# Performance work log

Hardware: AMD Instinct MI355X
Metric: run time of the kernel (lower is better)

Reference implementation:

```python
import jax, jax.numpy as jnp
import numpy as np

EPS = 1e-8
LN_EPS = 1e-5
PSCALE = 10.0
P = 8  # n_points


def _bb_frames(Xn, Xca, Xc):
    # Gram-Schmidt rigid frame from N, CA, C (AlphaFold rigids_from_3_points).
    v1 = Xc - Xca
    v2 = Xn - Xca
    e1 = v1 / jnp.sqrt(jnp.sum(v1 * v1, -1, keepdims=True) + EPS)
    u2 = v2 - e1 * jnp.sum(e1 * v2, -1, keepdims=True)
    e2 = u2 / jnp.sqrt(jnp.sum(u2 * u2, -1, keepdims=True) + EPS)
    e3 = jnp.cross(e1, e2)
    R = jnp.stack([e1, e2, e3], axis=-1)  # [B,N,3,3], columns are basis vectors
    t = Xca / PSCALE                      # scale_translation(1/position_scale)
    return R, t


def _layernorm(x, g, b):
    mu = jnp.mean(x, -1, keepdims=True)
    var = jnp.mean((x - mu) ** 2, -1, keepdims=True)
    return (x - mu) / jnp.sqrt(var + LN_EPS) * g + b


def setup_inputs() -> dict:
    key = jax.random.key(0)
    ks = jax.random.split(key, 24)
    B, N, K, D, H = 8, 512, 32, 128, 128
    msg_in = 2 * D + D + 9 * P  # 456
    s = 0.02
    inp = {
        "h_V": jax.random.normal(ks[0], (B, N, D), jnp.float32),
        "h_E": jax.random.normal(ks[1], (B, N, K, D), jnp.float32),
        "X": jax.random.normal(ks[2], (B, N, 3, 3), jnp.float32),
        "mask_V": jnp.ones((B, N), jnp.float32),
        "mask_attend": jnp.ones((B, N, K), jnp.float32),
        "Wp": jax.random.normal(ks[3], (D, P * 3), jnp.float32) * s,
        "bp": jnp.zeros((P * 3,), jnp.float32),
        "Wm1": jax.random.normal(ks[4], (msg_in, H), jnp.float32) * s,
        "bm1": jnp.zeros((H,), jnp.float32),
        "Wm2": jax.random.normal(ks[5], (H, H), jnp.float32) * s,
        "bm2": jnp.zeros((H,), jnp.float32),
        "Wm3": jax.random.normal(ks[6], (H, H), jnp.float32) * s,
        "bm3": jnp.zeros((H,), jnp.float32),
        "g1": jnp.ones((H,), jnp.float32),
        "be1": jnp.zeros((H,), jnp.float32),
        "Wd1": jax.random.normal(ks[7], (H, 4 * H), jnp.float32) * s,
        "bd1": jnp.zeros((4 * H,), jnp.float32),
        "Wd2": jax.random.normal(ks[8], (4 * H, H), jnp.float32) * s,
        "bd2": jnp.zeros((H,), jnp.float32),
        "g2": jnp.ones((H,), jnp.float32),
        "be2": jnp.zeros((H,), jnp.float32),
        "E_idx": jax.random.randint(ks[9], (B, N, K), 0, N, jnp.int32),
    }
    return inp


def reference(h_V, h_E, X, mask_V, mask_attend,
              Wp, bp, Wm1, bm1, Wm2, bm2, Wm3, bm3, g1, be1,
              Wd1, bd1, Wd2, bd2, g2, be2, E_idx):
    B, N, K = E_idx.shape
    R, t = _bb_frames(X[..., 0, :], X[..., 1, :], X[..., 2, :])
    # local points [B,N,P,3]
    p_local = (h_V @ Wp + bp).reshape(B, N, P, 3)
    # global points: R @ p + t
    p_global = jnp.einsum('bnij,bnpj->bnpi', R, p_local) + t[:, :, None, :]
    bidx = jnp.arange(B)[:, None, None]
    nbr_pg = p_global[bidx, E_idx]  # [B,N,K,P,3]
    nbr_hV = h_V[bidx, E_idx]       # [B,N,K,D]
    # distances in global frame
    diff = p_global[:, :, None] - nbr_pg
    npg_norm = jnp.sqrt(jnp.sum(diff * diff, -1) + EPS)  # [B,N,K,P]
    # neighbor points in local frame: R^T (q - t)
    q = nbr_pg - t[:, :, None, None, :]
    nbr_pl = jnp.einsum('bnij,bnkpi->bnkpj', R, q)       # [B,N,K,P,3]
    npl_norm = jnp.sqrt(jnp.sum(nbr_pl * nbr_pl, -1) + EPS)
    pl_norm = jnp.sqrt(jnp.sum(p_local * p_local, -1) + EPS)  # [B,N,P]

    D = h_V.shape[-1]
    node_expand = jnp.broadcast_to(h_V[:, :, None, :], (B, N, K, D))
    pl_flat = jnp.broadcast_to(p_local[:, :, None], (B, N, K, P, 3)).reshape(B, N, K, P * 3)
    pl_norm_e = jnp.broadcast_to(pl_norm[:, :, None, :], (B, N, K, P))
    msg_in = jnp.concatenate([
        node_expand, h_E, nbr_hV,
        pl_flat, pl_norm_e,
        nbr_pl.reshape(B, N, K, P * 3), npl_norm, npg_norm,
    ], axis=-1)

    # node_message_fn: 3-layer MLP with relu
    m = jax.nn.relu(msg_in @ Wm1 + bm1)
    m = jax.nn.relu(m @ Wm2 + bm2)
    m = m @ Wm3 + bm3
    m = m * mask_attend[..., None]
    node_m = jnp.mean(m, axis=-2)  # [B,N,H]

    h = _layernorm(h_V + node_m, g1, be1)  # dropout = identity (eval)
    dense = jax.nn.relu(h @ Wd1 + bd1) @ Wd2 + bd2
    h = _layernorm(h + dense, g2, be2)
    h = h * mask_V[..., None]
    return h, h_E
```

## Files before the change

### kernel.cpp

```cpp
#include <hip/hip_runtime.h>
#include <hip/hip_bf16.h>

typedef __hip_bfloat16 bf16;
typedef __attribute__((ext_vector_type(8))) short s16x8;
typedef __attribute__((ext_vector_type(4))) float f32x4;

#define DEV __device__ __forceinline__

DEV float us2f(unsigned short u){ return __uint_as_float(((unsigned int)u) << 16); }
DEV unsigned short f2us(float f){
    __hip_bfloat16 h = __float2bfloat16(f);
    unsigned short r; __builtin_memcpy(&r, &h, 2); return r;
}
DEV unsigned pack2(float a, float b){ return (unsigned)f2us(a) | ((unsigned)f2us(b) << 16); }

template<bool F32> DEV float ldf(const void* p, long i){
    if (F32) return reinterpret_cast<const float*>(p)[i];
    return us2f(reinterpret_cast<const unsigned short*>(p)[i]);
}
template<bool F32> DEV unsigned short ld16(const void* p, long i){
    if (F32) return f2us(reinterpret_cast<const float*>(p)[i]);
    return reinterpret_cast<const unsigned short*>(p)[i];
}

union U16x8 { uint4 u; s16x8 v; };

DEV bool is_f32(const void* maskV){
    return reinterpret_cast<const unsigned short*>(maskV)[0] != 0x3F80;
}

struct __align__(16) PreSmem {
    union __align__(16) {
        unsigned short lwT[128*40];
        struct {
            unsigned short lwp[24*132];
            float sX[2][9], sR[2][9], st3[2][3], spl[2][24], hvs[2][128];
        } pr;
    } u;
};

template<bool F32>
DEV void pre_prep(const void* hV, const void* X, const void* Wp, const void* bp,
                  float* pg, float* pl, float* pln, float* Rw, float* tw,
                  PreSmem& s, int bid, int tid)
{
    auto& pr = s.u.pr;
    for (int e = tid; e < 3072; e += 128) {
        int i = e / 24, j = e - i*24;
        pr.lwp[j*132 + i] = ld16<F32>(Wp, e);
    }
    const int wv = tid >> 6, ln = tid & 63;
    const int n = bid*2 + wv;
    if (ln < 9) pr.sX[wv][ln] = ldf<F32>(X, (long)n*9 + ln);
    for (int i = ln; i < 128; i += 64) pr.hvs[wv][i] = ldf<F32>(hV, (long)n*128 + i);
    __syncthreads();

    if (ln == 0) {
        float Nx=pr.sX[wv][0],Ny=pr.sX[wv][1],Nz=pr.sX[wv][2];
        float Ax=pr.sX[wv][3],Ay=pr.sX[wv][4],Az=pr.sX[wv][5];
        float Cx=pr.sX[wv][6],Cy=pr.sX[wv][7],Cz=pr.sX[wv][8];
        float v1x=Cx-Ax, v1y=Cy-Ay, v1z=Cz-Az;
        float v2x=Nx-Ax, v2y=Ny-Ay, v2z=Nz-Az;
        float r1 = 1.f/sqrtf(v1x*v1x+v1y*v1y+v1z*v1z + 1e-8f);
        float e1x=v1x*r1, e1y=v1y*r1, e1z=v1z*r1;
        float dp = e1x*v2x+e1y*v2y+e1z*v2z;
        float u2x=v2x-e1x*dp, u2y=v2y-e1y*dp, u2z=v2z-e1z*dp;
        float r2 = 1.f/sqrtf(u2x*u2x+u2y*u2y+u2z*u2z + 1e-8f);
        float e2x=u2x*r2, e2y=u2y*r2, e2z=u2z*r2;
        float e3x = e1y*e2z - e1z*e2y;
        float e3y = e1z*e2x - e1x*e2z;
        float e3z = e1x*e2y - e1y*e2x;
        pr.sR[wv][0]=e1x; pr.sR[wv][1]=e2x; pr.sR[wv][2]=e3x;
        pr.sR[wv][3]=e1y; pr.sR[wv][4]=e2y; pr.sR[wv][5]=e3y;
        pr.sR[wv][6]=e1z; pr.sR[wv][7]=e2z; pr.sR[wv][8]=e3z;
        pr.st3[wv][0]=Ax*0.1f; pr.st3[wv][1]=Ay*0.1f; pr.st3[wv][2]=Az*0.1f;
    }
    if (ln < 24) {
        float acc = ldf<F32>(bp, ln);
        const unsigned short* wr = &pr.lwp[ln*132];
        #pragma unroll
        for (int c=0;c<16;c++){
            #pragma unroll
            for (int k=0;k<8;k++)
                acc += pr.hvs[wv][c*8+k] * us2f(wr[c*8+k]);
        }
        pr.spl[wv][ln] = acc;
    }
    __syncthreads();

    if (ln < 24) {
        pl[n*24+ln] = pr.spl[wv][ln];
        int p = ln/3, c = ln - p*3;
        float g = pr.sR[wv][c*3+0]*pr.spl[wv][p*3+0] + pr.sR[wv][c*3+1]*pr.spl[wv][p*3+1]
                + pr.sR[wv][c*3+2]*pr.spl[wv][p*3+2] + pr.st3[wv][c];
        pg[n*24+ln] = g;
    }
    if (ln < 9) Rw[n*9+ln] = pr.sR[wv][ln];
    if (ln < 3) tw[n*3+ln] = pr.st3[wv][ln];
    if (ln < 8) {
        float a=pr.spl[wv][ln*3], b=pr.spl[wv][ln*3+1], c=pr.spl[wv][ln*3+2];
        pln[n*8+ln] = sqrtf(a*a+b*b+c*c + 1e-8f);
    }
}

template<bool F32>
DEV void pre_uv(const void* hV, const void* bm1, const void* Wm1,
                unsigned short* Uw, unsigned short* Vw,
                PreSmem& s, int r0, int tid)
{
    const int lane = tid & 63, w2 = tid >> 6;
    const int lm = lane & 15, quad = lane >> 4;

    s16x8 af[4];
    #pragma unroll
    for (int kc=0; kc<4; ++kc) {
        long src = (long)(r0 + lm)*128 + kc*32 + quad*8;
        U16x8 pk;
        if (F32) {
            const float4* vp = reinterpret_cast<const float4*>(reinterpret_cast<const float*>(hV) + src);
            float4 x = vp[0], y = vp[1];
            pk.u.x = pack2(x.x,x.y); pk.u.y = pack2(x.z,x.w);
            pk.u.z = pack2(y.x,y.y); pk.u.w = pack2(y.z,y.w);
        } else {
            pk.u = *reinterpret_cast<const uint4*>(reinterpret_cast<const unsigned short*>(hV) + src);
        }
        af[kc] = pk.v;
    }

    f32x4 accU[4], accV[4];
    #pragma unroll
    for (int nt=0; nt<4; ++nt) {
        float b0 = ldf<F32>(bm1, 64*w2 + nt*16 + lm);
        f32x4 iv = {b0,b0,b0,b0};
        accU[nt] = iv;
        f32x4 zv = {0.f,0.f,0.f,0.f};
        accV[nt] = zv;
    }

    for (int p=0; p<8; ++p) {
        int k0 = (p<4) ? p*32 : 256 + (p-4)*32;
        __syncthreads();
        for (int e = tid; e < 4096; e += 128) {
            int kk = e >> 7, c = e & 127;
            s.u.lwT[c*40 + kk] = ld16<F32>(Wm1, (long)k0*128 + e);
        }
        __syncthreads();
        s16x8 a = af[p & 3];
        #pragma unroll
        for (int nt=0; nt<4; ++nt) {
            s16x8 bf = *reinterpret_cast<const s16x8*>(&s.u.lwT[(64*w2 + nt*16 + lm)*40 + quad*8]);
            if (p < 4) accU[nt] = __builtin_amdgcn_mfma_f32_16x16x32_bf16(a, bf, accU[nt], 0,0,0);
            else       accV[nt] = __builtin_amdgcn_mfma_f32_16x16x32_bf16(a, bf, accV[nt], 0,0,0);
        }
    }
    #pragma unroll
    for (int nt=0; nt<4; ++nt)
        #pragma unroll
        for (int r=0; r<4; ++r) {
            long o = (long)(r0 + quad*4 + r)*128 + 64*w2 + nt*16 + lm;
            Uw[o] = f2us(accU[nt][r]);
            Vw[o] = f2us(accV[nt][r]);
        }
}

template<bool F32>
DEV void pre_wt(const void* Wm1, const void* Wm2, const void* Wm3,
                const void* Wd1, const void* Wd2,
                unsigned short* wt1, unsigned short* wt2, unsigned short* wt3,
                unsigned short* wd1T, unsigned short* wd2T, long t)
{
    if (t < 61440) {
        int k = (int)(t >> 7), h = (int)(t & 127);
        wt1[(long)h*480 + k] = (k < 456) ? ld16<F32>(Wm1, (long)k*128 + h) : (unsigned short)0;
    } else if (t < 77824) {
        long t2 = t - 61440; int k = (int)(t2 >> 7), h = (int)(t2 & 127);
        wt2[(long)h*128 + k] = ld16<F32>(Wm2, (long)k*128 + h);
    } else if (t < 94208) {
        long t2 = t - 77824; int k = (int)(t2 >> 7), h = (int)(t2 & 127);
        wt3[(long)h*128 + k] = ld16<F32>(Wm3, (long)k*128 + h);
    } else if (t < 159744) {
        long t2 = t - 94208; int k = (int)(t2 >> 9), n = (int)(t2 & 511);
        wd1T[(long)n*128 + k] = ld16<F32>(Wd1, (long)k*512 + n);
    } else {
        long t2 = t - 159744; int k = (int)(t2 >> 7), n = (int)(t2 & 127);
        wd2T[(long)n*512 + k] = ld16<F32>(Wd2, (long)k*128 + n);
    }
}

__global__ __launch_bounds__(128) void pre_k(
    const void* __restrict__ hV, const void* __restrict__ X,
    const void* __restrict__ Wp, const void* __restrict__ bp,
    const void* __restrict__ Wm1, const void* __restrict__ bm1,
    const void* __restrict__ Wm2, const void* __restrict__ Wm3,
    const void* __restrict__ Wd1, const void* __restrict__ Wd2,
    float* __restrict__ pg, float* __restrict__ pl, float* __restrict__ pln,
    float* __restrict__ Rw, float* __restrict__ tw,
    unsigned short* __restrict__ Uw, unsigned short* __restrict__ Vw,
    unsigned short* __restrict__ wt1, unsigned short* __restrict__ wt2,
    unsigned short* __restrict__ wt3, unsigned short* __restrict__ wd1T,
    unsigned short* __restrict__ wd2T, const void* __restrict__ maskV)
{
    __shared__ PreSmem s;
    int bid = blockIdx.x, tid = threadIdx.x;
    bool f32 = is_f32(maskV);
    if (bid < 2048) {
        if (f32) pre_prep<true >(hV,X,Wp,bp,pg,pl,pln,Rw,tw,s,bid,tid);
        else     pre_prep<false>(hV,X,Wp,bp,pg,pl,pln,Rw,tw,s,bid,tid);
    } else if (bid < 2304) {
        int r0 = (bid - 2048) * 16;
        if (f32) pre_uv<true >(hV,bm1,Wm1,Uw,Vw,s,r0,tid);
        else     pre_uv<false>(hV,bm1,Wm1,Uw,Vw,s,r0,tid);
    } else {
        long t = (long)(bid - 2304)*128 + tid;
        if (f32) pre_wt<true >(Wm1,Wm2,Wm3,Wd1,Wd2,wt1,wt2,wt3,wd1T,wd2T,t);
        else     pre_wt<false>(Wm1,Wm2,Wm3,Wd1,Wd2,wt1,wt2,wt3,wd1T,wd2T,t);
    }
}

#define ASTRIDE 40
#define MSTRIDE 136

struct __align__(16) Mp1Smem {
    union __align__(16) {
        unsigned short geo[3][64*ASTRIDE];
        unsigned short m[64*MSTRIDE];
    } u;
    int   sj[64];
    float smka[64];
    float spg[2][24], spl[2][24], spln[2][8], sR[2][9], st3[2][3];
    unsigned short sU[2*128];
};

template<bool F32>
DEV void mpnn1_body(
    const void* hV, const void* hE, const void* maskA,
    const void* bm2, const void* bm3, const int* Eidx,
    const float* pg, const float* pl, const float* pln,
    const float* Rw, const float* tw,
    const unsigned short* wt1, const unsigned short* wt2, const unsigned short* wt3,
    const unsigned short* Uw, const unsigned short* Vw,
    float* nodemsg, void* outE, Mp1Smem& sm, int n0, int tid)
{
    const int lane = tid & 63, w = tid >> 6;
    const int lm = lane & 15, quad = lane >> 4;

    if (tid < 64) { int l = tid >> 5;
        sm.sj[tid] = (((n0+l) >> 9) << 9) + Eidx[(long)(n0+l)*32 + (tid & 31)];
    } else { int t = tid - 64; int l = t >> 5;
        sm.smka[t] = ldf<F32>(maskA, (long)(n0+l)*32 + (t & 31));
    }
    if (tid < 48)        { sm.spg[tid/24][tid%24] = pg[(n0+tid/24)*24 + tid%24]; }
    else if (tid < 96)   { int t=tid-48; sm.spl[t/24][t%24] = pl[(n0+t/24)*24 + t%24]; }
    else if (tid < 112)  { int t=tid-96; sm.spln[t>>3][t&7]  = pln[(n0+(t>>3))*8 + (t&7)]; }
    if (tid < 18)        { sm.sR[tid/9][tid%9] = Rw[(n0+tid/9)*9 + tid%9]; }
    else if (tid < 24)   { int t=tid-18; sm.st3[t/3][t%3] = tw[(n0+t/3)*3 + t%3]; }
    for (int e = tid; e < 256; e += 128)
        sm.sU[e] = Uw[(long)(n0 + (e>>7))*128 + (e & 127)];
    __syncthreads();

    #pragma unroll
    for (int pass=0; pass<4; ++pass) {
        int v = tid + pass*128;
        int row = v >> 3, p = v & 7, nd = row >> 5;
        int j = sm.sj[row];
        float qx = pg[j*24 + p*3 + 0];
        float qy = pg[j*24 + p*3 + 1];
        float qz = pg[j*24 + p*3 + 2];
        float dx = sm.spg[nd][p*3+0]-qx, dy = sm.spg[nd][p*3+1]-qy, dz = sm.spg[nd][p*3+2]-qz;
        float npg = sqrtf(dx*dx+dy*dy+dz*dz + 1e-8f);
        float ux = qx - sm.st3[nd][0], uy = qy - sm.st3[nd][1], uz = qz - sm.st3[nd][2];
        float l0 = sm.sR[nd][0]*ux + sm.sR[nd][3]*uy + sm.sR[nd][6]*uz;
        float l1 = sm.sR[nd][1]*ux + sm.sR[nd][4]*uy + sm.sR[nd][7]*uz;
        float l2v= sm.sR[nd][2]*ux + sm.sR[nd][5]*uy + sm.sR[nd][8]*uz;
        float npl = sqrtf(l0*l0+l1*l1+l2v*l2v + 1e-8f);
        unsigned short* C0 = sm.u.geo[0];
        unsigned short* C1 = sm.u.geo[1];
        unsigned short* C2 = sm.u.geo[2];
        C0[row*ASTRIDE + p*3+0] = f2us(sm.spl[nd][p*3+0]);
        C0[row*ASTRIDE + p*3+1] = f2us(sm.spl[nd][p*3+1]);
        C0[row*ASTRIDE + p*3+2] = f2us(sm.spl[nd][p*3+2]);
        C0[row*ASTRIDE + 24+p]  = f2us(sm.spln[nd][p]);
        C1[row*ASTRIDE + p*3+0] = f2us(l0);
        C1[row*ASTRIDE + p*3+1] = f2us(l1);
        C1[row*ASTRIDE + p*3+2] = f2us(l2v);
        C1[row*ASTRIDE + 24+p]  = f2us(npl);
        C2[row*ASTRIDE + p]     = f2us(npg);
    }
    for (int z = tid; z < 64*24; z += 128) {
        int row = z / 24, col = 8 + (z % 24);
        sm.u.geo[2][row*ASTRIDE + col] = 0;
    }
    __syncthreads();

    const unsigned short* wr1[4];
    #pragma unroll
    for (int nt=0; nt<4; ++nt) wr1[nt] = wt1 + (long)(64*w + nt*16 + lm)*480 + quad*8;

    f32x4 acc[4][4];
    {
        f32x4 zv = {0.f,0.f,0.f,0.f};
        #pragma unroll
        for (int mt=0; mt<4; ++mt)
            #pragma unroll
            for (int nt=0; nt<4; ++nt) acc[mt][nt] = zv;
    }

    #pragma unroll
    for (int c=0; c<4; ++c) {
        s16x8 av[4];
        #pragma unroll
        for (int mt=0; mt<4; ++mt) {
            int row16 = 16*mt + lm, nd = mt >> 1;
            long src = ((long)(n0+nd)*32 + (row16&31))*128 + c*32 + quad*8;
            U16x8 pk;
            if (F32) {
                const float4* vp = reinterpret_cast<const float4*>(reinterpret_cast<const float*>(hE) + src);
                float4 x = vp[0], y = vp[1];
                if (w == 0) {
                    float4* d = reinterpret_cast<float4*>(reinterpret_cast<float*>(outE) + src);
                    d[0] = x; d[1] = y;
                }
                pk.u.x = pack2(x.x,x.y); pk.u.y = pack2(x.z,x.w);
                pk.u.z = pack2(y.x,y.y); pk.u.w = pack2(y.z,y.w);
            } else {
                pk.u = *reinterpret_cast<const uint4*>(reinterpret_cast<const unsigned short*>(hE) + src);
                if (w == 0)
                    *reinterpret_cast<uint4*>(reinterpret_cast<unsigned short*>(outE) + src) = pk.u;
            }
            av[mt] = pk.v;
        }
        #pragma unroll
        for (int nt=0; nt<4; ++nt) {
            s16x8 bf = *reinterpret_cast<const s16x8*>(wr1[nt] + (long)(c+4)*32);
            #pragma unroll
            for (int mt=0; mt<4; ++mt)
                acc[mt][nt] = __builtin_amdgcn_mfma_f32_16x16x32_bf16(av[mt], bf, acc[mt][nt], 0,0,0);
        }
    }
    #pragma unroll
    for (int c=0; c<3; ++c) {
        s16x8 av[4];
        #pragma unroll
        for (int mt=0; mt<4; ++mt)
            av[mt] = *reinterpret_cast<const s16x8*>(&sm.u.geo[c][(16*mt+lm)*ASTRIDE + quad*8]);
        #pragma unroll
        for (int nt=0; nt<4; ++nt) {
            s16x8 bf = *reinterpret_cast<const s16x8*>(wr1[nt] + (long)(c+12)*32);
            #pragma unroll
            for (int mt=0; mt<4; ++mt)
                acc[mt][nt] = __builtin_amdgcn_mfma_f32_16x16x32_bf16(av[mt], bf, acc[mt][nt], 0,0,0);
        }
    }
    __syncthreads();

    #pragma unroll
    for (int mt=0; mt<4; ++mt)
        #pragma unroll
        for (int nt=0; nt<4; ++nt)
            #pragma unroll
            for (int r=0; r<4; ++r)
                sm.u.m[(16*mt + quad*4 + r)*MSTRIDE + 64*w + nt*16 + lm]
                    = f2us(acc[mt][nt][r]);

    const int row = tid >> 1, ch = tid & 1;
    const int jv = sm.sj[row];
    const unsigned short* vrow = Vw + (long)jv*128 + ch*64;
    uint4 pv[8];
    #pragma unroll
    for (int b=0;b<8;++b) pv[b] = *reinterpret_cast<const uint4*>(vrow + b*8);
    __syncthreads();

    {
        unsigned short* mrow = &sm.u.m[row*MSTRIDE + ch*64];
        const unsigned short* urow = &sm.sU[(row>>5)*128 + ch*64];
        #pragma unroll
        for (int b=0;b<8;++b) {
            U16x8 vm; vm.u = *reinterpret_cast<const uint4*>(mrow + b*8);
            U16x8 vv; vv.u = pv[b];
            float f[8];
            #pragma unroll
            for (int i=0;i<8;++i)
                f[i] = fmaxf(us2f((unsigned short)vm.v[i]) + us2f((unsigned short)vv.v[i])
                             + us2f(urow[b*8+i]), 0.f);
            uint4 o;
            o.x = pack2(f[0],f[1]); o.y = pack2(f[2],f[3]);
            o.z = pack2(f[4],f[5]); o.w = pack2(f[6],f[7]);
            *reinterpret_cast<uint4*>(mrow + b*8) = o;
        }
    }
    __syncthreads();

    #pragma unroll
    for (int nt=0; nt<4; ++nt) {
        float b0 = ldf<F32>(bm2, 64*w + nt*16 + lm);
        f32x4 iv = {b0,b0,b0,b0};
        #pragma unroll
        for (int mt=0; mt<4; ++mt) acc[mt][nt] = iv;
    }
    #pragma unroll
    for (int kc=0; kc<4; ++kc) {
        s16x8 av[4];
        #pragma unroll
        for (int mt=0; mt<4; ++mt)
            av[mt] = *reinterpret_cast<const s16x8*>(&sm.u.m[(16*mt+lm)*MSTRIDE + kc*32 + quad*8]);
        #pragma unroll
        for (int nt=0; nt<4; ++nt) {
            s16x8 bf = *reinterpret_cast<const s16x8*>(&wt2[(long)(64*w + nt*16 + lm)*128 + kc*32 + quad*8]);
            #pragma unroll
            for (int mt=0; mt<4; ++mt)
                acc[mt][nt] = __builtin_amdgcn_mfma_f32_16x16x32_bf16(av[mt], bf, acc[mt][nt], 0,0,0);
        }
    }
    __syncthreads();

    #pragma unroll
    for (int mt=0; mt<4; ++mt)
        #pragma unroll
        for (int nt=0; nt<4; ++nt)
            #pragma unroll
            for (int r=0; r<4; ++r)
                sm.u.m[(16*mt + quad*4 + r)*MSTRIDE + 64*w + nt*16 + lm]
                    = f2us(fmaxf(acc[mt][nt][r], 0.f));
    __syncthreads();

    #pragma unroll
    for (int nt=0; nt<4; ++nt) {
        float b0 = ldf<F32>(bm3, 64*w + nt*16 + lm);
        f32x4 iv = {b0,b0,b0,b0};
        #pragma unroll
        for (int mt=0; mt<4; ++mt) acc[mt][nt] = iv;
    }
    #pragma unroll
    for (int kc=0; kc<4; ++kc) {
        s16x8 av[4];
        #pragma unroll
        for (int mt=0; mt<4; ++mt)
            av[mt] = *reinterpret_cast<const s16x8*>(&sm.u.m[(16*mt+lm)*MSTRIDE + kc*32 + quad*8]);
        #pragma unroll
        for (int nt=0; nt<4; ++nt) {
            s16x8 bf = *reinterpret_cast<const s16x8*>(&wt3[(long)(64*w + nt*16 + lm)*128 + kc*32 + quad*8]);
            #pragma unroll
            for (int mt=0; mt<4; ++mt)
                acc[mt][nt] = __builtin_amdgcn_mfma_f32_16x16x32_bf16(av[mt], bf, acc[mt][nt], 0,0,0);
        }
    }

    #pragma unroll
    for (int nt=0; nt<4; ++nt) {
        float s0 = 0.f, s1 = 0.f;
        #pragma unroll
        for (int r=0; r<4; ++r) {
            s0 += acc[0][nt][r] * sm.smka[     quad*4 + r]
                + acc[1][nt][r] * sm.smka[16 + quad*4 + r];
            s1 += acc[2][nt][r] * sm.smka[32 + quad*4 + r]
                + acc[3][nt][r] * sm.smka[48 + quad*4 + r];
        }
        s0 += __shfl_xor(s0, 16); s0 += __shfl_xor(s0, 32);
        s1 += __shfl_xor(s1, 16); s1 += __shfl_xor(s1, 32);
        if (lane < 16) {
            nodemsg[(long)(n0  )*128 + 64*w + nt*16 + lane] = s0;
            nodemsg[(long)(n0+1)*128 + 64*w + nt*16 + lane] = s1;
        }
    }
}

__global__ __launch_bounds__(128) void mpnn1_k(
    const void* __restrict__ hV, const void* __restrict__ hE,
    const void* __restrict__ maskV, const void* __restrict__ maskA,
    const void* __restrict__ bm2, const void* __restrict__ bm3,
    const int* __restrict__ Eidx,
    const float* __restrict__ pg, const float* __restrict__ pl,
    const float* __restrict__ pln, const float* __restrict__ Rw,
    const float* __restrict__ tw,
    const unsigned short* __restrict__ wt1, const unsigned short* __restrict__ wt2,
    const unsigned short* __restrict__ wt3,
    const unsigned short* __restrict__ Uw, const unsigned short* __restrict__ Vw,
    float* __restrict__ nodemsg, void* __restrict__ dout)
{
    __shared__ Mp1Smem sm;
    int n0 = blockIdx.x * 2, tid = threadIdx.x;
    if (is_f32(maskV)) {
        void* outE = reinterpret_cast<float*>(dout) + 524288;
        mpnn1_body<true >(hV,hE,maskA,bm2,bm3,Eidx,pg,pl,pln,Rw,tw,wt1,wt2,wt3,Uw,Vw,nodemsg,outE,sm,n0,tid);
    } else {
        void* outE = reinterpret_cast<unsigned short*>(dout) + 524288;
        mpnn1_body<false>(hV,hE,maskA,bm2,bm3,Eidx,pg,pl,pln,Rw,tw,wt1,wt2,wt3,Uw,Vw,nodemsg,outE,sm,n0,tid);
    }
}

#define TSTRIDE 520

struct __align__(16) FfnSmem {
    unsigned short x1[16*MSTRIDE];
    union __align__(16) {
        unsigned short t1[16*TSTRIDE];
        float yf[16*132];
    } u;
};

template<bool F32>
DEV void ffn_body(const void* hV, const void* maskV, const float* nodemsg,
                  const void* g1, const void* be1, const void* bd1, const void* bd2,
                  const void* g2, const void* be2,
                  const unsigned short* wd1T, const unsigned short* wd2T,
                  void* out, FfnSmem& sm, int n0, int tid)
{
    const int lane = tid & 63, w = tid >> 6;
    const int lm = lane & 15, quad = lane >> 4;

    {
        const int r = tid >> 4, c0 = (tid & 15) * 8;
        const long nb = (long)(n0 + r)*128;
        float xv[8];
        float s1 = 0.f, s2 = 0.f;
        #pragma unroll
        for (int j=0; j<8; ++j) {
            float v = ldf<F32>(hV, nb + c0 + j) + nodemsg[nb + c0 + j] * (1.f/32.f);
            xv[j] = v; s1 += v; s2 += v*v;
        }
        s1 += __shfl_xor(s1,1); s1 += __shfl_xor(s1,2);
        s1 += __shfl_xor(s1,4); s1 += __shfl_xor(s1,8);
        s2 += __shfl_xor(s2,1); s2 += __shfl_xor(s2,2);
        s2 += __shfl_xor(s2,4); s2 += __shfl_xor(s2,8);
        float mu = s1 * (1.f/128.f);
        float var = s2 * (1.f/128.f) - mu*mu;
        float rs = 1.f/sqrtf(var + 1e-5f);
        #pragma unroll
        for (int j=0; j<8; ++j) {
            int c = c0 + j;
            sm.x1[r*MSTRIDE + c] = f2us((xv[j]-mu)*rs*ldf<F32>(g1, c) + ldf<F32>(be1, c));
        }
    }
    __syncthreads();

    {
        f32x4 t1a[8];
        #pragma unroll
        for (int nt=0; nt<8; ++nt) {
            float b0 = ldf<F32>(bd1, 128*w + nt*16 + lm);
            f32x4 iv = {b0,b0,b0,b0};
            t1a[nt] = iv;
        }
        #pragma unroll
        for (int kc=0; kc<4; ++kc) {
            s16x8 a = *reinterpret_cast<const s16x8*>(&sm.x1[lm*MSTRIDE + kc*32 + quad*8]);
            #pragma unroll
            for (int nt=0; nt<8; ++nt) {
                s16x8 bf = *reinterpret_cast<const s16x8*>(&wd1T[(long)(128*w + nt*16 + lm)*128 + kc*32 + quad*8]);
                t1a[nt] = __builtin_amdgcn_mfma_f32_16x16x32_bf16(a, bf, t1a[nt], 0,0,0);
            }
        }
        #pragma unroll
        for (int nt=0; nt<8; ++nt)
            #pragma unroll
            for (int r=0; r<4; ++r)
                sm.u.t1[(quad*4 + r)*TSTRIDE + 128*w + nt*16 + lm] = f2us(fmaxf(t1a[nt][r], 0.f));
    }
    __syncthreads();

    f32x4 yacc[2];
    #pragma unroll
    for (int nt=0; nt<2; ++nt) {
        float b0 = ldf<F32>(bd2, 32*w + nt*16 + lm);
        f32x4 iv = {b0,b0,b0,b0};
        yacc[nt] = iv;
    }
    #pragma unroll
    for (int kc=0; kc<16; ++kc) {
        s16x8 a = *reinterpret_cast<const s16x8*>(&sm.u.t1[lm*TSTRIDE + kc*32 + quad*8]);
        #pragma unroll
        for (int nt=0; nt<2; ++nt) {
            s16x8 bf = *reinterpret_cast<const s16x8*>(&wd2T[(long)(32*w + nt*16 + lm)*512 + kc*32 + quad*8]);
            yacc[nt] = __builtin_amdgcn_mfma_f32_16x16x32_bf16(a, bf, yacc[nt], 0,0,0);
        }
    }
    __syncthreads();

    #pragma unroll
    for (int nt=0; nt<2; ++nt)
        #pragma unroll
        for (int r=0; r<4; ++r) {
            int rr = quad*4 + r, c = 32*w + nt*16 + lm;
            sm.u.yf[rr*132 + c] = yacc[nt][r] + us2f(sm.x1[rr*MSTRIDE + c]);
        }
    __syncthreads();

    {
        const int r = tid >> 4, c0 = (tid & 15) * 8;
        float yv[8];
        float s1 = 0.f, s2 = 0.f;
        #pragma unroll
        for (int j=0; j<8; ++j) {
            float v = sm.u.yf[r*132 + c0 + j];
            yv[j] = v; s1 += v; s2 += v*v;
        }
        s1 += __shfl_xor(s1,1); s1 += __shfl_xor(s1,2);
        s1 += __shfl_xor(s1,4); s1 += __shfl_xor(s1,8);
        s2 += __shfl_xor(s2,1); s2 += __shfl_xor(s2,2);
        s2 += __shfl_xor(s2,4); s2 += __shfl_xor(s2,8);
        float mu = s1 * (1.f/128.f);
        float var = s2 * (1.f/128.f) - mu*mu;
        float rs = 1.f/sqrtf(var + 1e-5f);
        float mv = ldf<F32>(maskV, n0 + r);
        const long ob = (long)(n0 + r)*128 + c0;
        #pragma unroll
        for (int j=0; j<8; ++j) {
            int c = c0 + j;
            float v = ((yv[j]-mu)*rs*ldf<F32>(g2, c) + ldf<F32>(be2, c)) * mv;
            if (F32) reinterpret_cast<float*>(out)[ob + j] = v;
            else     reinterpret_cast<unsigned short*>(out)[ob + j] = f2us(v);
        }
    }
}

__global__ __launch_bounds__(256) void ffn_k(
    const void* __restrict__ hV, const void* __restrict__ maskV,
    const float* __restrict__ nodemsg,
    const void* __restrict__ g1, const void* __restrict__ be1,
    const void* __restrict__ bd1, const void* __restrict__ bd2,
    const void* __restrict__ g2, const void* __restrict__ be2,
    const unsigned short* __restrict__ wd1T, const unsigned short* __restrict__ wd2T,
    void* __restrict__ out)
{
    __shared__ FfnSmem sm;
    int n0 = blockIdx.x * 16, tid = threadIdx.x;
    if (is_f32(maskV))
        ffn_body<true >(hV,maskV,nodemsg,g1,be1,bd1,bd2,g2,be2,wd1T,wd2T,out,sm,n0,tid);
    else
        ffn_body<false>(hV,maskV,nodemsg,g1,be1,bd1,bd2,g2,be2,wd1T,wd2T,out,sm,n0,tid);
}

extern "C" void kernel_launch(void* const* d_in, const int* in_sizes, int n_in,
                              void* d_out, int out_size, void* d_ws, size_t ws_size,
                              hipStream_t stream)
{
    const void* hV    = d_in[0];
    const void* hE    = d_in[1];
    const void* X     = d_in[2];
    const void* maskV = d_in[3];
    const void* maskA = d_in[4];
    const void* Wp    = d_in[5];
    const void* bp    = d_in[6];
    const void* Wm1   = d_in[7];
    const void* bm1   = d_in[8];
    const void* Wm2   = d_in[9];
    const void* bm2   = d_in[10];
    const void* Wm3   = d_in[11];
    const void* bm3   = d_in[12];
    const void* g1    = d_in[13];
    const void* be1   = d_in[14];
    const void* Wd1   = d_in[15];
    const void* bd1   = d_in[16];
    const void* Wd2   = d_in[17];
    const void* bd2   = d_in[18];
    const void* g2    = d_in[19];
    const void* be2   = d_in[20];
    const int*  Eidx  = (const int*)d_in[21];

    float* ws = (float*)d_ws;
    float* pg  = ws;
    float* pl  = ws + 98304;
    float* pln = ws + 196608;
    float* Rw  = ws + 229376;
    float* tw  = ws + 266240;
    float* nm  = ws + 278528;
    unsigned short* wt1  = (unsigned short*)(ws + 802816);
    unsigned short* wt2  = wt1 + 61440;
    unsigned short* wt3  = wt2 + 16384;
    unsigned short* wd1T = wt3 + 16384;
    unsigned short* wd2T = wd1T + 65536;
    unsigned short* Uw   = wd2T + 65536;
    unsigned short* Vw   = Uw + 524288;

    pre_k<<<4064, 128, 0, stream>>>(hV, X, Wp, bp, Wm1, bm1, Wm2, Wm3, Wd1, Wd2,
                                    pg, pl, pln, Rw, tw, Uw, Vw,
                                    wt1, wt2, wt3, wd1T, wd2T, maskV);

    mpnn1_k<<<2048, 128, 0, stream>>>(hV, hE, maskV, maskA, bm2, bm3, Eidx,
                                      pg, pl, pln, Rw, tw, wt1, wt2, wt3,
                                      Uw, Vw, nm, d_out);

    ffn_k<<<256, 256, 0, stream>>>(hV, maskV, nm, g1, be1, bd1, bd2, g2, be2,
                                   wd1T, wd2T, d_out);
}
```

Before: 245.0 us.

## Move h_E passthrough copy into pre kernel and stage bf16 h_E copy

Adds 2048 blocks to the pre kernel that copy h_E into the output and, when the workspace is large enough, also write a bf16 copy of h_E. mpnn1 then reads the half-size bf16 copy instead of fp32 h_E and no longer does the output copy inside its GEMM loop. This takes store traffic and fp32 loads off the critical MLP kernel, but it adds an extra full write of bf16 h_E plus the passthrough copy in pre_k. Total memory traffic may not drop, since h_E is read in fp32 once and then re-read as bf16.

```diff
diff --git a/kernel.cpp b/kernel.cpp
--- a/kernel.cpp
+++ b/kernel.cpp
@@ -38,6 +38,38 @@
         } pr;
     } u;
 };
+
+template<bool F32>
+DEV void pre_copy(const void* hE, void* outE, unsigned short* hEb, int cb, int tid)
+{
+    if (F32) {
+        const float* src = reinterpret_cast<const float*>(hE) + (long)cb*8192;
+        float* dst = reinterpret_cast<float*>(outE) + (long)cb*8192;
+        unsigned short* hb = hEb ? hEb + (long)cb*8192 : nullptr;
+        #pragma unroll
+        for (int u=0; u<8; ++u) {
+            long o = (long)u*1024 + tid*8;
+            float4 x = *reinterpret_cast<const float4*>(src + o);
+            float4 y = *reinterpret_cast<const float4*>(src + o + 4);
+            *reinterpret_cast<float4*>(dst + o)     = x;
+            *reinterpret_cast<float4*>(dst + o + 4) = y;
+            if (hb) {
+                uint4 p;
+                p.x = pack2(x.x,x.y); p.y = pack2(x.z,x.w);
+                p.z = pack2(y.x,y.y); p.w = pack2(y.z,y.w);
+                *reinterpret_cast<uint4*>(hb + o) = p;
+            }
+        }
+    } else {
+        const unsigned short* src = reinterpret_cast<const unsigned short*>(hE) + (long)cb*8192;
+        unsigned short* dst = reinterpret_cast<unsigned short*>(outE) + (long)cb*8192;
+        #pragma unroll
+        for (int u=0; u<8; ++u) {
+            long o = (long)u*1024 + tid*8;
+            *reinterpret_cast<uint4*>(dst + o) = *reinterpret_cast<const uint4*>(src + o);
+        }
+    }
+}
 
 template<bool F32>
 DEV void pre_prep(const void* hV, const void* X, const void* Wp, const void* bp,
@@ -189,6 +221,7 @@
 
 __global__ __launch_bounds__(128) void pre_k(
     const void* __restrict__ hV, const void* __restrict__ X,
+    const void* __restrict__ hE,
     const void* __restrict__ Wp, const void* __restrict__ bp,
     const void* __restrict__ Wm1, const void* __restrict__ bm1,
     const void* __restrict__ Wm2, const void* __restrict__ Wm3,
@@ -198,20 +231,25 @@
     unsigned short* __restrict__ Uw, unsigned short* __restrict__ Vw,
     unsigned short* __restrict__ wt1, unsigned short* __restrict__ wt2,
     unsigned short* __restrict__ wt3, unsigned short* __restrict__ wd1T,
-    unsigned short* __restrict__ wd2T, const void* __restrict__ maskV)
+    unsigned short* __restrict__ wd2T,
+    unsigned short* __restrict__ hEb, void* __restrict__ dout,
+    const void* __restrict__ maskV)
 {
     __shared__ PreSmem s;
     int bid = blockIdx.x, tid = threadIdx.x;
     bool f32 = is_f32(maskV);
     if (bid < 2048) {
-        if (f32) pre_prep<true >(hV,X,Wp,bp,pg,pl,pln,Rw,tw,s,bid,tid);
-        else     pre_prep<false>(hV,X,Wp,bp,pg,pl,pln,Rw,tw,s,bid,tid);
-    } else if (bid < 2304) {
-        int r0 = (bid - 2048) * 16;
+        if (f32) pre_copy<true >(hE, reinterpret_cast<float*>(dout) + 524288, hEb, bid, tid);
+        else     pre_copy<false>(hE, reinterpret_cast<unsigned short*>(dout) + 524288, hEb, bid, tid);
+    } else if (bid < 4096) {
+        if (f32) pre_prep<true >(hV,X,Wp,bp,pg,pl,pln,Rw,tw,s,bid-2048,tid);
+        else     pre_prep<false>(hV,X,Wp,bp,pg,pl,pln,Rw,tw,s,bid-2048,tid);
+    } else if (bid < 4352) {
+        int r0 = (bid - 4096) * 16;
         if (f32) pre_uv<true >(hV,bm1,Wm1,Uw,Vw,s,r0,tid);
         else     pre_uv<false>(hV,bm1,Wm1,Uw,Vw,s,r0,tid);
     } else {
-        long t = (long)(bid - 2304)*128 + tid;
+        long t = (long)(bid - 4352)*128 + tid;
         if (f32) pre_wt<true >(Wm1,Wm2,Wm3,Wd1,Wd2,wt1,wt2,wt3,wd1T,wd2T,t);
         else     pre_wt<false>(Wm1,Wm2,Wm3,Wd1,Wd2,wt1,wt2,wt3,wd1T,wd2T,t);
     }
@@ -231,15 +269,15 @@
     unsigned short sU[2*128];
 };
 
-template<bool F32>
+template<bool F32, bool AF32>
 DEV void mpnn1_body(
-    const void* hV, const void* hE, const void* maskA,
+    const void* hEsrc, const void* maskA,
     const void* bm2, const void* bm3, const int* Eidx,
     const float* pg, const float* pl, const float* pln,
     const float* Rw, const float* tw,
     const unsigned short* wt1, const unsigned short* wt2, const unsigned short* wt3,
     const unsigned short* Uw, const unsigned short* Vw,
-    float* nodemsg, void* outE, Mp1Smem& sm, int n0, int tid)
+    float* nodemsg, Mp1Smem& sm, int n0, int tid)
 {
     const int lane = tid & 63, w = tid >> 6;
     const int lm = lane & 15, quad = lane >> 4;
@@ -313,19 +351,13 @@
             int row16 = 16*mt + lm, nd = mt >> 1;
             long src = ((long)(n0+nd)*32 + (row16&31))*128 + c*32 + quad*8;
             U16x8 pk;
-            if (F32) {
-                const float4* vp = reinterpret_cast<const float4*>(reinterpret_cast<const float*>(hE) + src);
+            if (AF32) {
+                const float4* vp = reinterpret_cast<const float4*>(reinterpret_cast<const float*>(hEsrc) + src);
                 float4 x = vp[0], y = vp[1];
-                if (w == 0) {
-                    float4* d = reinterpret_cast<float4*>(reinterpret_cast<float*>(outE) + src);
-                    d[0] = x; d[1] = y;
-                }
                 pk.u.x = pack2(x.x,x.y); pk.u.y = pack2(x.z,x.w);
                 pk.u.z = pack2(y.x,y.y); pk.u.w = pack2(y.z,y.w);
             } else {
-                pk.u = *reinterpret_cast<const uint4*>(reinterpret_cast<const unsigned short*>(hE) + src);
-                if (w == 0)
-                    *reinterpret_cast<uint4*>(reinterpret_cast<unsigned short*>(outE) + src) = pk.u;
+                pk.u = *reinterpret_cast<const uint4*>(reinterpret_cast<const unsigned short*>(hEsrc) + src);
             }
             av[mt] = pk.v;
         }
@@ -465,7 +497,7 @@
 }
 
 __global__ __launch_bounds__(128) void mpnn1_k(
-    const void* __restrict__ hV, const void* __restrict__ hE,
+    const void* __restrict__ hE, const unsigned short* __restrict__ hEb,
     const void* __restrict__ maskV, const void* __restrict__ maskA,
     const void* __restrict__ bm2, const void* __restrict__ bm3,
     const int* __restrict__ Eidx,
@@ -475,16 +507,17 @@
     const unsigned short* __restrict__ wt1, const unsigned short* __restrict__ wt2,
     const unsigned short* __restrict__ wt3,
     const unsigned short* __restrict__ Uw, const unsigned short* __restrict__ Vw,
-    float* __restrict__ nodemsg, void* __restrict__ dout)
+    float* __restrict__ nodemsg, int heb_ok)
 {
     __shared__ Mp1Smem sm;
     int n0 = blockIdx.x * 2, tid = threadIdx.x;
     if (is_f32(maskV)) {
-        void* outE = reinterpret_cast<float*>(dout) + 524288;
-        mpnn1_body<true >(hV,hE,maskA,bm2,bm3,Eidx,pg,pl,pln,Rw,tw,wt1,wt2,wt3,Uw,Vw,nodemsg,outE,sm,n0,tid);
+        if (heb_ok)
+            mpnn1_body<true ,false>(hEb,maskA,bm2,bm3,Eidx,pg,pl,pln,Rw,tw,wt1,wt2,wt3,Uw,Vw,nodemsg,sm,n0,tid);
+        else
+            mpnn1_body<true ,true >(hE, maskA,bm2,bm3,Eidx,pg,pl,pln,Rw,tw,wt1,wt2,wt3,Uw,Vw,nodemsg,sm,n0,tid);
     } else {
-        void* outE = reinterpret_cast<unsigned short*>(dout) + 524288;
-        mpnn1_body<false>(hV,hE,maskA,bm2,bm3,Eidx,pg,pl,pln,Rw,tw,wt1,wt2,wt3,Uw,Vw,nodemsg,outE,sm,n0,tid);
+        mpnn1_body<false,false>(hE, maskA,bm2,bm3,Eidx,pg,pl,pln,Rw,tw,wt1,wt2,wt3,Uw,Vw,nodemsg,sm,n0,tid);
     }
 }
 
@@ -671,14 +704,18 @@
     unsigned short* wd2T = wd1T + 65536;
     unsigned short* Uw   = wd2T + 65536;
     unsigned short* Vw   = Uw + 524288;
-
-    pre_k<<<4064, 128, 0, stream>>>(hV, X, Wp, bp, Wm1, bm1, Wm2, Wm3, Wd1, Wd2,
+    unsigned short* hEb  = (unsigned short*)(ws + 1439744);
+    int heb_ok = (ws_size >= 9828352ull * 4ull) ? 1 : 0;
+    unsigned short* hEb_arg = heb_ok ? hEb : nullptr;
+
+    pre_k<<<6112, 128, 0, stream>>>(hV, X, hE, Wp, bp, Wm1, bm1, Wm2, Wm3, Wd1, Wd2,
                                     pg, pl, pln, Rw, tw, Uw, Vw,
-                                    wt1, wt2, wt3, wd1T, wd2T, maskV);
-
-    mpnn1_k<<<2048, 128, 0, stream>>>(hV, hE, maskV, maskA, bm2, bm3, Eidx,
+                                    wt1, wt2, wt3, wd1T, wd2T,
+                                    hEb_arg, d_out, maskV);
+
+    mpnn1_k<<<2048, 128, 0, stream>>>(hE, hEb_arg, maskV, maskA, bm2, bm3, Eidx,
                                       pg, pl, pln, Rw, tw, wt1, wt2, wt3,
-                                      Uw, Vw, nm, d_out);
+                                      Uw, Vw, nm, heb_ok);
 
     ffn_k<<<256, 256, 0, stream>>>(hV, maskV, nm, g1, be1, bd1, bd2, g2, be2,
                                    wd1T, wd2T, d_out);
```

Result: slower. 259.8 us (+6.0%).
